# Kernel optimization log

Measured on AMD Instinct MI355X. Metric: run time of the kernel, lower is better.

Reference implementation:

```python
import jax, jax.numpy as jnp
import numpy as np

T, N, L, H, COND, VOCAB = 64, 1024, 16, 256, 64, 100
HC = H + 1  # task_encoder hidden = hidden_size + 1
STATE = 1 + 1 + H + L + L  # a, v, h, a_probs, p


def gru_step(x, h, w_ih, w_hh, b_ih, b_hh):
    # PyTorch GRU/GRUCell gate math
    gi = x @ w_ih.T + b_ih
    gh = h @ w_hh.T + b_hh
    ir, iz, ig = jnp.split(gi, 3, axis=-1)
    hr, hz, hg = jnp.split(gh, 3, axis=-1)
    r = jax.nn.sigmoid(ir + hr)
    z = jax.nn.sigmoid(iz + hz)
    n = jnp.tanh(ig + r * hg)
    return (1.0 - z) * n + z * h


def setup_inputs():
    ks = jax.random.split(jax.random.key(0), 20)
    g = lambda i, sh: jax.random.normal(ks[i], sh, jnp.float32) * 0.05
    return {
        "condition": jax.random.normal(ks[0], (T, N, COND), jnp.float32),
        "lines": jax.random.randint(ks[1], (N, L), 0, VOCAB),
        "actions": jax.random.randint(ks[2], (T, N), 0, L),
        "rnn_hxs": jnp.zeros((N, STATE), jnp.float32),
        "emb": g(3, (VOCAB, H)),
        "w_ih_enc": g(4, (3 * HC, H)), "w_hh_enc": g(5, (3 * HC, HC)),
        "b_ih_enc": g(6, (3 * HC,)), "b_hh_enc": g(7, (3 * HC,)),
        "W1": g(8, (H, COND + H)), "b1": g(9, (H,)),
        "W2": g(10, (H, H)), "b2": g(11, (H,)),
        "w_ih_cell": g(12, (3 * H, H)), "w_hh_cell": g(13, (3 * H, H)),
        "b_ih_cell": g(14, (3 * H,)), "b_hh_cell": g(15, (3 * H,)),
        "Wa": g(16, (H, H)), "ba": g(17, (H,)),
        "Wc": g(18, (1, H)), "bc": g(19, (1,)),
    }


def _forward(condition, rnn_hxs, emb, w_ih_enc, w_hh_enc, b_ih_enc, b_hh_enc,
             W1, b1, W2, b2, w_ih_cell, w_hh_cell, b_ih_cell, b_hh_cell,
             Wa, ba, Wc, bc, lines, actions):
    n, l = lines.shape
    M = emb[lines]                     # [N, L, H]
    seq = jnp.transpose(M, (1, 0, 2))  # [L, N, H]
    idx = jnp.arange(l)

    # backward encoder: single scan over reversed sequence (outputs are causal,
    # so they equal torch's task_encoder(backward_input[:i]) for every i)
    def bstep(h, x):
        h2 = gru_step(x, h, w_ih_enc, w_hh_enc, b_ih_enc, b_hh_enc)
        return h2, h2
    _, B = jax.lax.scan(bstep, jnp.zeros((n, HC), M.dtype), seq[::-1])  # [L, N, HC]

    # forward encoder from every start i, batched over i with a start mask
    def fstep(carry, xj):
        x, j = xj
        h2 = gru_step(x, carry, w_ih_enc, w_hh_enc, b_ih_enc, b_hh_enc)  # [L(i), N, HC]
        h2 = jnp.where((j >= idx)[:, None, None], h2, carry)
        return h2, h2
    _, Fo = jax.lax.scan(fstep, jnp.zeros((l, n, HC), M.dtype), (seq, idx))  # [j, i, N, HC]
    Fo = jnp.transpose(Fo, (1, 0, 2, 3))                                     # [i, j, N, HC]

    # keys[i] = cat(flip(B[:i]), F_i)  ->  entry j<i is B[i-1-j], else forward enc
    bidx = jnp.clip(idx[:, None] - 1 - idx[None, :], 0, l - 1)  # [i, j]
    Kfull = jnp.where((idx[None, :] < idx[:, None])[:, :, None, None], B[bidx], Fo)
    Kfull = jnp.transpose(Kfull, (2, 0, 1, 3))  # [N, i, j, HC]
    K = Kfull[..., :H].sum(axis=1)              # [N, L, H]
    C = Kfull[..., H]                           # [N, i, j]

    _a, _v, h, _ap, p = jnp.split(rnn_hxs, [1, 2, 2 + H, 2 + H + l], axis=-1)
    new_ep = jnp.all(rnn_hxs == 0.0, axis=-1)
    p = p.at[:, 0].set(jnp.where(new_ep, 1.0, p[:, 0]))

    def step(carry, xs):
        h, p = carry
        cond_t, a_t = xs
        r = jnp.einsum('nl,nlh->nh', p, M)
        x = jnp.concatenate([cond_t, r], axis=-1)
        x = jax.nn.relu(x @ W1.T + b1)
        x = jax.nn.relu(x @ W2.T + b2)
        h = gru_step(x, h, w_ih_cell, w_hh_cell, b_ih_cell, b_hh_cell)
        k = h @ Wa.T + ba
        c = jnp.einsum('ni,nij->nj', p, C)
        w = jnp.einsum('nlh,nh->nl', K, k)
        probs = jax.nn.softmax(w * c, axis=-1)
        p_new = jax.nn.one_hot(a_t, l, dtype=h.dtype)  # actions >= 0 -> no resampling
        v = h @ Wc.T + bc
        out = jnp.concatenate([a_t[:, None].astype(h.dtype), v, h, probs, p_new], axis=-1)
        return (h, p_new), out

    _, hx = jax.lax.scan(step, (h, p), (condition, actions))  # [T, N, STATE]
    return hx


def reference(condition, lines, actions, rnn_hxs, emb, w_ih_enc, w_hh_enc, b_ih_enc, b_hh_enc, W1, b1, W2, b2, w_ih_cell, w_hh_cell, b_ih_cell, b_hh_cell, Wa, ba, Wc, bc):
    hx = _forward(condition, rnn_hxs, emb, w_ih_enc, w_hh_enc, b_ih_enc, b_hh_enc,
                  W1, b1, W2, b2, w_ih_cell, w_hh_cell, b_ih_cell, b_hh_cell,
                  Wa, ba, Wc, bc, lines, actions)
    return hx, hx[-1:]
```

## Files before the change

kernel.cpp:

```cpp
#include <hip/hip_runtime.h>
#include <hip/hip_bf16.h>
#include <cstddef>

#define T_ 64
#define N_ 1024
#define L_ 16
#define H_ 256
#define STATE_ 290
#define EKSTR 296

typedef short s16x8 __attribute__((ext_vector_type(8)));
typedef float f32x4 __attribute__((ext_vector_type(4)));
typedef ushort us4 __attribute__((ext_vector_type(4)));
typedef ushort us8 __attribute__((ext_vector_type(8)));
#define MFMA16 __builtin_amdgcn_mfma_f32_16x16x32_bf16

#define BAR() asm volatile("s_waitcnt lgkmcnt(0)\n\ts_barrier" ::: "memory")

__device__ __forceinline__ float b2f(ushort u){ return __uint_as_float(((unsigned)u) << 16); }
__device__ __forceinline__ ushort f2b(float f){
  unsigned x = __float_as_uint(f);
  return (ushort)((x + 0x7FFFu + ((x >> 16) & 1u)) >> 16);
}
__device__ __forceinline__ float gruh(float gir,float giz,float gig,
                                      float ghr,float ghz,float ghg,float hp){
  float r = 1.f/(1.f + __expf(-(gir + ghr)));
  float z = 1.f/(1.f + __expf(-(giz + ghz)));
  float ex = __expf(2.f*(gig + r*ghg));
  float g = 1.f - 2.f/(ex + 1.f);
  return (1.f - z)*g + z*hp;
}

__global__ void prep_all(
    const float* __restrict__ wih_e, const float* __restrict__ whh_e,
    ushort* __restrict__ wihe_p, ushort* __restrict__ whhe_p,
    const float* __restrict__ wih_c, const float* __restrict__ whh_c,
    ushort* __restrict__ wihc_p, ushort* __restrict__ whhc_p,
    const float* __restrict__ bih_c, const float* __restrict__ bhh_c, float* __restrict__ cb,
    const float* __restrict__ W1, ushort* __restrict__ W1b,
    const float* __restrict__ W2, ushort* __restrict__ W2b,
    const float* __restrict__ Wa, ushort* __restrict__ WaTb){
  int b = blockIdx.x, t = threadIdx.x;
  if (b < 832) {
    int idx = b*256 + t;
    int d = idx >> 8, c = idx & 255;
    int tile = d >> 4, uu = d & 15;
    int k = tile/3, p = tile - 3*k;
    int hc = k*16 + uu;
    bool ok = (tile < 51) && (hc < 257);
    wihe_p[idx] = ok ? f2b(wih_e[(size_t)(p*257 + hc)*256 + c]) : (ushort)0;
  } else if (b < 1768) {
    int idx = (b-832)*256 + t;
    int d = idx / 288, c = idx - d*288;
    int tile = d >> 4, uu = d & 15;
    int k = tile/3, p = tile - 3*k;
    int hc = k*16 + uu;
    bool ok = (tile < 51) && (hc < 257) && (c < 257);
    whhe_p[idx] = ok ? f2b(whh_e[(size_t)(p*257 + hc)*257 + c]) : (ushort)0;
  } else if (b < 2536) {
    int idx = (b-1768)*256 + t;
    int d = idx >> 8, c = idx & 255;
    int tile = d >> 4, uu = d & 15;
    int k = tile/3, p = tile - 3*k;
    wihc_p[idx] = f2b(wih_c[(size_t)(p*256 + k*16 + uu)*256 + c]);
  } else if (b < 3304) {
    int idx = (b-2536)*256 + t;
    int d = idx >> 8, c = idx & 255;
    int tile = d >> 4, uu = d & 15;
    int k = tile/3, p = tile - 3*k;
    whhc_p[idx] = f2b(whh_c[(size_t)(p*256 + k*16 + uu)*256 + c]);
  } else if (b < 3307) {
    int d = (b-3304)*256 + t;
    if (d < 768) {
      int tile = d >> 4, uu = d & 15;
      int k = tile/3, p = tile - 3*k;
      int src = p*256 + k*16 + uu;
      cb[d] = bih_c[src] + (p < 2 ? bhh_c[src] : 0.f);
    }
  } else if (b < 3627) {
    int idx = (b-3307)*256 + t;
    W1b[idx] = f2b(W1[idx]);
  } else if (b < 3883) {
    int idx = (b-3627)*256 + t;
    W2b[idx] = f2b(W2[idx]);
  } else {
    int m = b - 3883;
    WaTb[(size_t)t*256 + m] = f2b(Wa[(size_t)m*256 + t]);
  }
}

__global__ void emb_init_r0(
    const int* __restrict__ lines, const float* __restrict__ emb, const float* __restrict__ hxs,
    ushort* __restrict__ Mbf, float* __restrict__ hbuf, float* __restrict__ p0,
    float* __restrict__ r0v){
  __shared__ ushort Ms[16][256];
  __shared__ float p0s[16];
  __shared__ int ls[16];
  __shared__ int nz;
  int n = blockIdx.x, t = threadIdx.x;
  if (t == 0) nz = 0;
  if (t < 16) ls[t] = lines[n*16 + t];
  __syncthreads();
  #pragma unroll
  for (int l = 0; l < 16; ++l) {
    ushort v = f2b(emb[(size_t)ls[l]*256 + t]);
    Ms[l][t] = v;
    Mbf[((size_t)n*16 + l)*256 + t] = v;
  }
  for (int c = t; c < STATE_; c += 256)
    if (hxs[(size_t)n*STATE_ + c] != 0.f) atomicOr(&nz, 1);
  __syncthreads();
  bool new_ep = (nz == 0);
  hbuf[(size_t)n*256 + t] = hxs[(size_t)n*STATE_ + 2 + t];
  if (t < 16) {
    float pv = hxs[(size_t)n*STATE_ + 2 + 256 + 16 + t];
    if (t == 0 && new_ep) pv = 1.f;
    p0[n*16 + t] = pv;
    p0s[t] = pv;
  }
  __syncthreads();
  float s = 0.f;
  #pragma unroll
  for (int l = 0; l < 16; ++l) s += p0s[l]*b2f(Ms[l][t]);
  r0v[(size_t)n*256 + t] = s;
}

__global__ void build_xcat8(const float* __restrict__ cond, const int* __restrict__ act,
                            const float* __restrict__ r0v, const ushort* __restrict__ Mbf,
                            ushort* __restrict__ xcat){
  int idx = blockIdx.x*256 + threadIdx.x;
  if (idx >= T_*N_*40) return;
  int kc = idx % 40;
  int row = idx / 40;
  int n = row & 1023, t = row >> 10;
  us8 v;
  if (kc < 8) {
    const float* cp = cond + (size_t)row*64 + kc*8;
    #pragma unroll
    for (int i = 0; i < 8; ++i) v[i] = f2b(cp[i]);
  } else if (t == 0) {
    const float* rp = r0v + (size_t)n*256 + (kc-8)*8;
    #pragma unroll
    for (int i = 0; i < 8; ++i) v[i] = f2b(rp[i]);
  } else {
    int a = act[(size_t)(t-1)*1024 + n];
    v = *(const us8*)(Mbf + ((size_t)n*16 + a)*256 + (kc-8)*8);
  }
  *(us8*)(xcat + (size_t)idx*8) = v;
}

template<int RELU>
__global__ __launch_bounds__(256) void gemm_mfma(
    const ushort* __restrict__ A, const ushort* __restrict__ W,
    const float* __restrict__ bias, ushort* __restrict__ out,
    int Kd, int ldo){
  __shared__ __align__(16) ushort Ws[64*328];
  int lane = threadIdx.x & 63, wv = threadIdx.x >> 6;
  int u = lane & 15, g4 = lane >> 4;
  int br = blockIdx.x*64 + wv*16;
  int bm = blockIdx.y*64;
  int ldw = Kd + 8;
  for (int i = threadIdx.x; i < 8*Kd; i += 256) {
    int e = i*8;
    int row = e / Kd, col = e - row*Kd;
    *(us8*)&Ws[row*ldw + col] = *(const us8*)(W + (size_t)(bm + row)*Kd + col);
  }
  __syncthreads();
  const ushort* Arow = A + (size_t)(br + u)*Kd + g4*8;
  f32x4 acc0 = {0,0,0,0}, acc1 = {0,0,0,0}, acc2 = {0,0,0,0}, acc3 = {0,0,0,0};
  for (int k0 = 0; k0 < Kd; k0 += 32) {
    s16x8 av = *(const s16x8*)(Arow + k0);
    s16x8 b0 = *(const s16x8*)&Ws[( 0 + u)*ldw + k0 + g4*8];
    s16x8 b1 = *(const s16x8*)&Ws[(16 + u)*ldw + k0 + g4*8];
    s16x8 b2 = *(const s16x8*)&Ws[(32 + u)*ldw + k0 + g4*8];
    s16x8 b3 = *(const s16x8*)&Ws[(48 + u)*ldw + k0 + g4*8];
    acc0 = MFMA16(av, b0, acc0, 0,0,0);
    acc1 = MFMA16(av, b1, acc1, 0,0,0);
    acc2 = MFMA16(av, b2, acc2, 0,0,0);
    acc3 = MFMA16(av, b3, acc3, 0,0,0);
  }
  f32x4 ac[4] = {acc0, acc1, acc2, acc3};
  #pragma unroll
  for (int mt = 0; mt < 4; ++mt) {
    int col = bm + mt*16 + u;
    float b = bias ? bias[col] : 0.f;
    #pragma unroll
    for (int r = 0; r < 4; ++r) {
      float v = ac[mt][r] + b;
      if (RELU) v = fmaxf(v, 0.f);
      out[(size_t)(br + g4*4 + r)*ldo + col] = f2b(v);
    }
  }
}

__global__ __launch_bounds__(512) __attribute__((amdgpu_waves_per_eu(2, 2))) void enc_all(
    const ushort* __restrict__ GiAll, const ushort* __restrict__ Wh,
    const float* __restrict__ bih, const float* __restrict__ bhh,
    float* __restrict__ Km, float* __restrict__ Cm, ushort* __restrict__ Bbf){
  __shared__ __align__(16) ushort hbf[2][80][EKSTR];
  __shared__ __align__(16) ushort gis[2][2][4][832];
  int tid = threadIdx.x, lane = tid & 63, wv = tid >> 6;
  int u = lane & 15, g4 = lane >> 4;
  int nb = blockIdx.x * 4;
  for (int i = tid; i < 2*80*EKSTR; i += 512) ((ushort*)hbf)[i] = 0;
  #pragma unroll
  for (int i0 = 0; i0 < 4; ++i0) {
    int i = tid + i0*512;
    if (i < 1664) {
      int flat = i*4;
      int fb = flat / 3328, rem = flat - fb*3328;
      int nl = rem / 832, k = rem - nl*832;
      int row = (nb+nl)*16 + (fb ? 15 : 0);
      *(us4*)&gis[0][fb][nl][k] = *(const us4*)(GiAll + (size_t)row*832 + k);
    }
  }
  BAR();
  int cur = 0;
  for (int j = 0; j < 16; ++j) {
    if (j < 15) {
      #pragma unroll
      for (int i0 = 0; i0 < 4; ++i0) {
        int i = tid + i0*512;
        if (i < 1664) {
          int flat = i*4;
          int fb = flat / 3328, rem = flat - fb*3328;
          int nl = rem / 832, k = rem - nl*832;
          int row = (nb+nl)*16 + (fb ? (14-j) : (j+1));
          *(us4*)&gis[cur^1][fb][nl][k] = *(const us4*)(GiAll + (size_t)row*832 + k);
        }
      }
    }
    #pragma unroll 1
    for (int tt = 0; tt < 2; ++tt) {
      int kt = 2*wv + tt;
      f32x4 acc[5][3];
      #pragma unroll
      for (int rt = 0; rt < 5; ++rt) {
        acc[rt][0] = (f32x4){0,0,0,0};
        acc[rt][1] = (f32x4){0,0,0,0};
        acc[rt][2] = (f32x4){0,0,0,0};
      }
      #pragma unroll
      for (int q = 0; q < 9; ++q) {
        int off = q*32 + g4*8;
        s16x8 w0 = *(const s16x8*)(Wh + (size_t)((3*kt+0)*16 + u)*288 + off);
        s16x8 w1 = *(const s16x8*)(Wh + (size_t)((3*kt+1)*16 + u)*288 + off);
        s16x8 w2 = *(const s16x8*)(Wh + (size_t)((3*kt+2)*16 + u)*288 + off);
        #pragma unroll
        for (int rt = 0; rt < 5; ++rt) {
          if (rt < 4 && rt*4 > j) continue;
          s16x8 av = *(const s16x8*)&hbf[cur][rt*16 + u][off];
          acc[rt][0] = MFMA16(av, w0, acc[rt][0], 0,0,0);
          acc[rt][1] = MFMA16(av, w1, acc[rt][1], 0,0,0);
          acc[rt][2] = MFMA16(av, w2, acc[rt][2], 0,0,0);
        }
      }
      int c = kt*16 + u;
      float bi0 = bih[c], bi1 = bih[257+c], bi2 = bih[514+c];
      float bh0 = bhh[c], bh1 = bhh[257+c], bh2 = bhh[514+c];
      float kmP[4] = {0.f, 0.f, 0.f, 0.f};
      #pragma unroll
      for (int rt = 0; rt < 4; ++rt) {
        int ii = rt*4 + g4;
        if (rt*4 <= j && ii <= j) {
          #pragma unroll
          for (int r = 0; r < 4; ++r) {
            int rowl = rt*16 + g4*4 + r;
            const ushort* gp = &gis[cur][0][r][3*kt*16];
            float hp = b2f(hbf[cur][rowl][c]);
            float h2 = gruh(b2f(gp[u]) + bi0, b2f(gp[16+u]) + bi1, b2f(gp[32+u]) + bi2,
                            acc[rt][0][r] + bh0, acc[rt][1][r] + bh1,
                            acc[rt][2][r] + bh2, hp);
            hbf[cur^1][rowl][c] = f2b(h2);
            kmP[r] += h2;
          }
        }
      }
      #pragma unroll
      for (int r = 0; r < 4; ++r) {
        float s = kmP[r];
        s += __shfl_xor(s, 16, 64);
        s += __shfl_xor(s, 32, 64);
        if (g4 == 0) Km[((size_t)(nb+r)*16 + j)*256 + c] = s;
      }
      if (g4 == 0) {
        #pragma unroll
        for (int r = 0; r < 4; ++r) {
          const ushort* gp = &gis[cur][1][r][3*kt*16];
          float hp = b2f(hbf[cur][64 + r][c]);
          float h2 = gruh(b2f(gp[u]) + bi0, b2f(gp[16+u]) + bi1, b2f(gp[32+u]) + bi2,
                          acc[4][0][r] + bh0, acc[4][1][r] + bh1,
                          acc[4][2][r] + bh2, hp);
          hbf[cur^1][64 + r][c] = f2b(h2);
          Bbf[((size_t)j*1024 + nb + r)*288 + c] = f2b(h2);
        }
      }
    }
    if (wv < 5) {
      int rt = wv;
      bool go = (rt == 4) || (rt*4 <= j);
      if (go) {
        f32x4 a0 = {0,0,0,0}, a1 = {0,0,0,0}, a2 = {0,0,0,0};
        #pragma unroll
        for (int q = 0; q < 9; ++q) {
          int off = q*32 + g4*8;
          s16x8 w0 = *(const s16x8*)(Wh + (size_t)(48*16 + u)*288 + off);
          s16x8 w1 = *(const s16x8*)(Wh + (size_t)(49*16 + u)*288 + off);
          s16x8 w2 = *(const s16x8*)(Wh + (size_t)(50*16 + u)*288 + off);
          s16x8 av = *(const s16x8*)&hbf[cur][rt*16 + u][off];
          a0 = MFMA16(av, w0, a0, 0,0,0);
          a1 = MFMA16(av, w1, a1, 0,0,0);
          a2 = MFMA16(av, w2, a2, 0,0,0);
        }
        if (u == 0) {
          float bi0 = bih[256], bi1 = bih[513], bi2 = bih[770];
          float bh0 = bhh[256], bh1 = bhh[513], bh2 = bhh[770];
          if (rt < 4) {
            int ii = rt*4 + g4;
            if (ii <= j) {
              #pragma unroll
              for (int r = 0; r < 4; ++r) {
                int rowl = rt*16 + g4*4 + r;
                const ushort* gp = &gis[cur][0][r][768];
                float hp = b2f(hbf[cur][rowl][256]);
                float h2 = gruh(b2f(gp[0]) + bi0, b2f(gp[16]) + bi1, b2f(gp[32]) + bi2,
                                a0[r] + bh0, a1[r] + bh1, a2[r] + bh2, hp);
                hbf[cur^1][rowl][256] = f2b(h2);
                Cm[(size_t)(nb+r)*256 + ii*16 + j] = h2;
              }
            }
          } else if (g4 == 0) {
            #pragma unroll
            for (int r = 0; r < 4; ++r) {
              const ushort* gp = &gis[cur][1][r][768];
              float hp = b2f(hbf[cur][64 + r][256]);
              float h2 = gruh(b2f(gp[0]) + bi0, b2f(gp[16]) + bi1, b2f(gp[32]) + bi2,
                              a0[r] + bh0, a1[r] + bh1, a2[r] + bh2, hp);
              hbf[cur^1][64 + r][256] = f2b(h2);
              Bbf[((size_t)j*1024 + nb + r)*288 + 256] = f2b(h2);
            }
          }
        }
      }
    }
    BAR();
    cur ^= 1;
  }
}

__global__ void accum_wb(const ushort* __restrict__ Bbf, const float* __restrict__ Km,
                         ushort* __restrict__ Kmbf, float* __restrict__ Cm,
                         const float* __restrict__ ba, float* __restrict__ wbv){
  __shared__ float kms[16][257];
  int n = blockIdx.x, c = threadIdx.x;
  float s = 0.f;
  for (int jj = 15; jj >= 0; --jj) {
    if (jj < 15) s += b2f(Bbf[((size_t)(14-jj)*1024 + n)*288 + c]);
    size_t o = ((size_t)n*16 + jj)*256 + c;
    float v = Km[o] + s;
    Kmbf[o] = f2b(v);
    kms[jj][c] = v;
  }
  int i = c >> 4, j = c & 15;
  if (i > j) Cm[(size_t)n*256 + i*16 + j] = b2f(Bbf[((size_t)(i-1-j)*1024 + n)*288 + 256]);
  __syncthreads();
  int l = c >> 4, lane16 = c & 15;
  float t = 0.f;
  for (int m = lane16; m < 256; m += 16) t += kms[l][m]*ba[m];
  t += __shfl_down(t, 8, 16); t += __shfl_down(t, 4, 16);
  t += __shfl_down(t, 2, 16); t += __shfl_down(t, 1, 16);
  if (lane16 == 0) wbv[n*16 + l] = t;
}

__global__ __launch_bounds__(512) __attribute__((amdgpu_waves_per_eu(2, 2))) void cell_chunk(
    const ushort* __restrict__ Gi, const ushort* __restrict__ Wh,
    const float* __restrict__ bhh, const float* __restrict__ hbuf,
    int t0, ushort* __restrict__ hcT, float* __restrict__ out){
  __shared__ __align__(16) ushort hbf[2][16][266];
  __shared__ __align__(16) ushort gis[2][16][768];
  int tid = threadIdx.x, lane = tid & 63, wv = tid >> 6;
  int u = lane & 15, g4 = lane >> 4;
  int n0 = blockIdx.x * 16;
  int ktA = wv, ktB = wv + 8;
  int cA = ktA*16 + u, cB = ktB*16 + u;
  s16x8 WA0[8], WA1[8], WA2[8], WB0[8], WB1[8], WB2[8];
  #pragma unroll
  for (int q = 0; q < 8; ++q) {
    int off = q*32 + g4*8;
    WA0[q] = *(const s16x8*)(Wh + (size_t)((3*ktA+0)*16 + u)*256 + off);
    WA1[q] = *(const s16x8*)(Wh + (size_t)((3*ktA+1)*16 + u)*256 + off);
    WA2[q] = *(const s16x8*)(Wh + (size_t)((3*ktA+2)*16 + u)*256 + off);
    WB0[q] = *(const s16x8*)(Wh + (size_t)((3*ktB+0)*16 + u)*256 + off);
    WB1[q] = *(const s16x8*)(Wh + (size_t)((3*ktB+1)*16 + u)*256 + off);
    WB2[q] = *(const s16x8*)(Wh + (size_t)((3*ktB+2)*16 + u)*256 + off);
  }
  float bhgA = bhh[512 + cA], bhgB = bhh[512 + cB];
  if (t0 == 0) {
    for (int i = tid; i < 16*256; i += 512) {
      int rr = i >> 8, cc = i & 255;
      hbf[0][rr][cc] = f2b(hbuf[(size_t)(n0 + rr)*256 + cc]);
    }
  } else {
    for (int i = tid; i < 16*256; i += 512) {
      int rr = i >> 8, cc = i & 255;
      hbf[0][rr][cc] = hcT[((size_t)(t0-1)*1024 + n0 + rr)*256 + cc];
    }
  }
  for (int i = tid; i < 1536; i += 512)
    *(us8*)&((ushort*)gis[0])[i*8] = *(const us8*)(Gi + (size_t)n0*768 + i*8);
  BAR();
  int cur = 0;
  for (int s = 0; s < 16; ++s) {
    int t = t0 + s;
    if (s < 15) {
      const ushort* src = Gi + (size_t)(s+1)*1024*768 + (size_t)n0*768;
      for (int i = tid; i < 1536; i += 512)
        *(us8*)&((ushort*)gis[cur^1])[i*8] = *(const us8*)(src + i*8);
    }
    f32x4 a0={0,0,0,0},a1={0,0,0,0},a2={0,0,0,0};
    f32x4 b0={0,0,0,0},b1={0,0,0,0},b2={0,0,0,0};
    #pragma unroll
    for (int q = 0; q < 8; ++q) {
      s16x8 ah = *(const s16x8*)&hbf[cur][u][q*32 + g4*8];
      a0 = MFMA16(ah, WA0[q], a0, 0,0,0);
      a1 = MFMA16(ah, WA1[q], a1, 0,0,0);
      a2 = MFMA16(ah, WA2[q], a2, 0,0,0);
      b0 = MFMA16(ah, WB0[q], b0, 0,0,0);
      b1 = MFMA16(ah, WB1[q], b1, 0,0,0);
      b2 = MFMA16(ah, WB2[q], b2, 0,0,0);
    }
    #pragma unroll
    for (int r = 0; r < 4; ++r) {
      int row = g4*4 + r;
      const ushort* gr = &gis[cur][row][0];
      {
        float gir = b2f(gr[3*ktA*16 + u]);
        float giz = b2f(gr[3*ktA*16 + 16 + u]);
        float gig = b2f(gr[3*ktA*16 + 32 + u]);
        float hp  = b2f(hbf[cur][row][cA]);
        float rr2 = 1.f/(1.f + __expf(-(gir + a0[r])));
        float zz  = 1.f/(1.f + __expf(-(giz + a1[r])));
        float ex  = __expf(2.f*(gig + rr2*(a2[r] + bhgA)));
        float gg  = 1.f - 2.f/(ex + 1.f);
        float h2  = (1.f - zz)*gg + zz*hp;
        ushort hb = f2b(h2);
        hbf[cur^1][row][cA] = hb;
        hcT[((size_t)t*1024 + n0 + row)*256 + cA] = hb;
        out[((size_t)t*1024 + n0 + row)*STATE_ + 2 + cA] = h2;
        if (t == 63) out[((size_t)64*1024 + n0 + row)*STATE_ + 2 + cA] = h2;
      }
      {
        float gir = b2f(gr[3*ktB*16 + u]);
        float giz = b2f(gr[3*ktB*16 + 16 + u]);
        float gig = b2f(gr[3*ktB*16 + 32 + u]);
        float hp  = b2f(hbf[cur][row][cB]);
        float rr2 = 1.f/(1.f + __expf(-(gir + b0[r])));
        float zz  = 1.f/(1.f + __expf(-(giz + b1[r])));
        float ex  = __expf(2.f*(gig + rr2*(b2[r] + bhgB)));
        float gg  = 1.f - 2.f/(ex + 1.f);
        float h2  = (1.f - zz)*gg + zz*hp;
        ushort hb = f2b(h2);
        hbf[cur^1][row][cB] = hb;
        hcT[((size_t)t*1024 + n0 + row)*256 + cB] = hb;
        out[((size_t)t*1024 + n0 + row)*STATE_ + 2 + cB] = h2;
        if (t == 63) out[((size_t)64*1024 + n0 + row)*STATE_ + 2 + cB] = h2;
      }
    }
    BAR();
    cur ^= 1;
  }
}

__global__ __launch_bounds__(256) void attn_v(
    const ushort* __restrict__ Ktl, const ushort* __restrict__ hcT,
    const float* __restrict__ wbv, const float* __restrict__ Cm,
    const float* __restrict__ p0, const int* __restrict__ act,
    const float* __restrict__ Wc, const float* __restrict__ bc,
    float* __restrict__ out){
  __shared__ float WcS[256];
  int n = blockIdx.x;
  int tid = threadIdx.x;
  WcS[tid] = Wc[tid];
  __syncthreads();
  int lane = tid & 63, wv = tid >> 6;
  int u = lane & 15, g4 = lane >> 4;
  int t0 = wv*16;
  const ushort* Ka = Ktl + ((size_t)n*16 + u)*256 + g4*8;
  const ushort* Hb = hcT + ((size_t)(t0 + u)*1024 + n)*256 + g4*8;
  f32x4 acc = {0,0,0,0};
  float vp = 0.f;
  #pragma unroll
  for (int q = 0; q < 8; ++q) {
    s16x8 av = *(const s16x8*)(Ka + q*32);
    s16x8 bv = *(const s16x8*)(Hb + q*32);
    acc = MFMA16(av, bv, acc, 0,0,0);
    #pragma unroll
    for (int j = 0; j < 8; ++j) vp += b2f((ushort)bv[j]) * WcS[q*32 + g4*8 + j];
  }
  vp += __shfl_xor(vp, 16, 64);
  vp += __shfl_xor(vp, 32, 64);
  float vfin = vp + bc[0];
  int t = t0 + u;
  float ps[4];
  if (t == 0) {
    #pragma unroll
    for (int r = 0; r < 4; ++r) {
      float catt = 0.f;
      for (int i = 0; i < 16; ++i) catt += p0[n*16 + i]*Cm[(size_t)n*256 + i*16 + g4*4 + r];
      ps[r] = (acc[r] + wbv[n*16 + g4*4 + r]) * catt;
    }
  } else {
    int ap = act[(size_t)(t-1)*1024 + n];
    #pragma unroll
    for (int r = 0; r < 4; ++r)
      ps[r] = (acc[r] + wbv[n*16 + g4*4 + r]) * Cm[(size_t)n*256 + ap*16 + g4*4 + r];
  }
  float mx = fmaxf(fmaxf(ps[0], ps[1]), fmaxf(ps[2], ps[3]));
  mx = fmaxf(mx, __shfl_xor(mx, 16, 64));
  mx = fmaxf(mx, __shfl_xor(mx, 32, 64));
  float e[4], se = 0.f;
  #pragma unroll
  for (int r = 0; r < 4; ++r) { e[r] = __expf(ps[r] - mx); se += e[r]; }
  se += __shfl_xor(se, 16, 64);
  se += __shfl_xor(se, 32, 64);
  float inv = 1.f/se;
  int a = act[(size_t)t*1024 + n];
  size_t ro = ((size_t)t*1024 + n)*STATE_;
  if (g4 == 0) { out[ro] = (float)a; out[ro + 1] = vfin; }
  #pragma unroll
  for (int r = 0; r < 4; ++r) {
    out[ro + 258 + g4*4 + r] = e[r]*inv;
    out[ro + 274 + g4*4 + r] = (g4*4 + r == a) ? 1.f : 0.f;
  }
  if (t == 63) {
    size_t r2 = ((size_t)64*1024 + n)*STATE_;
    if (g4 == 0) { out[r2] = (float)a; out[r2 + 1] = vfin; }
    #pragma unroll
    for (int r = 0; r < 4; ++r) {
      out[r2 + 258 + g4*4 + r] = e[r]*inv;
      out[r2 + 274 + g4*4 + r] = (g4*4 + r == a) ? 1.f : 0.f;
    }
  }
}

extern "C" void kernel_launch(void* const* d_in, const int* in_sizes, int n_in,
                              void* d_out, int out_size, void* d_ws, size_t ws_size,
                              hipStream_t stream){
  (void)in_sizes; (void)n_in; (void)out_size; (void)ws_size;
  const float* cond  = (const float*)d_in[0];
  const int*   lines = (const int*)  d_in[1];
  const int*   act   = (const int*)  d_in[2];
  const float* hxs   = (const float*)d_in[3];
  const float* emb   = (const float*)d_in[4];
  const float* wih_e = (const float*)d_in[5];
  const float* whh_e = (const float*)d_in[6];
  const float* bih_e = (const float*)d_in[7];
  const float* bhh_e = (const float*)d_in[8];
  const float* W1    = (const float*)d_in[9];
  const float* b1    = (const float*)d_in[10];
  const float* W2    = (const float*)d_in[11];
  const float* b2    = (const float*)d_in[12];
  const float* wih_c = (const float*)d_in[13];
  const float* whh_c = (const float*)d_in[14];
  const float* bih_c = (const float*)d_in[15];
  const float* bhh_c = (const float*)d_in[16];
  const float* Wa    = (const float*)d_in[17];
  const float* ba    = (const float*)d_in[18];
  const float* Wc    = (const float*)d_in[19];
  const float* bc    = (const float*)d_in[20];
  float* out = (float*)d_out;

  char* base = (char*)d_ws;
  ushort* Mbf    = (ushort*)(base + 0);
  ushort* Bbf    = (ushort*)(base + 8388608);
  float*  Km     = (float*) (base + 17825792);
  ushort* Kmbf   = (ushort*)(base + 34603008);
  ushort* xcat   = (ushort*)(base + 8388608);
  ushort* x2     = (ushort*)(base + 8388608);
  ushort* hcT    = (ushort*)(base + 8388608);
  ushort* GiAll  = (ushort*)(base + 50331648);
  ushort* x1     = (ushort*)(base + 50331648);
  ushort* GiC0   = (ushort*)(base + 50331648);
  ushort* GiC1   = (ushort*)(base + 75497472);
  ushort* Ktl    = (ushort*)(base + 100663296);
  float*  Cm     = (float*) (base + 109051904);
  float*  hbuf   = (float*) (base + 110100480);
  float*  p0     = (float*) (base + 111149056);
  float*  r0v    = (float*) (base + 111214592);
  float*  wbv    = (float*) (base + 112263168);
  ushort* wihe_p = (ushort*)(base + 112328704);
  ushort* whhe_p = (ushort*)(base + 112754688);
  ushort* wihc_p = (ushort*)(base + 113233920);
  ushort* whhc_p = (ushort*)(base + 113627136);
  ushort* W1b    = (ushort*)(base + 114020352);
  ushort* W2b    = (ushort*)(base + 114184192);
  ushort* WaTb   = (ushort*)(base + 114315264);
  float*  cbias  = (float*) (base + 114446336);

  prep_all<<<4139, 256, 0, stream>>>(wih_e, whh_e, wihe_p, whhe_p,
                                     wih_c, whh_c, wihc_p, whhc_p,
                                     bih_c, bhh_c, cbias, W1, W1b, W2, W2b, Wa, WaTb);
  emb_init_r0<<<1024, 256, 0, stream>>>(lines, emb, hxs, Mbf, hbuf, p0, r0v);

  gemm_mfma<0><<<dim3(256, 13), 256, 0, stream>>>(Mbf, wihe_p, nullptr, GiAll, 256, 832);
  enc_all<<<256, 512, 0, stream>>>(GiAll, whhe_p, bih_e, bhh_e, Km, Cm, Bbf);
  accum_wb<<<1024, 256, 0, stream>>>(Bbf, Km, Kmbf, Cm, ba, wbv);
  gemm_mfma<0><<<dim3(256, 4), 256, 0, stream>>>(Kmbf, WaTb, nullptr, Ktl, 256, 256);

  build_xcat8<<<10240, 256, 0, stream>>>(cond, act, r0v, Mbf, xcat);
  gemm_mfma<1><<<dim3(1024, 4), 256, 0, stream>>>(xcat, W1b, b1, x1, 320, 256);
  gemm_mfma<1><<<dim3(1024, 4), 256, 0, stream>>>(x1, W2b, b2, x2, 256, 256);

  ushort* gic[2] = {GiC0, GiC1};
  gemm_mfma<0><<<dim3(256, 12), 256, 0, stream>>>(x2 + (size_t)0*16384*256, wihc_p, cbias, gic[0], 256, 768);
  gemm_mfma<0><<<dim3(256, 12), 256, 0, stream>>>(x2 + (size_t)1*16384*256, wihc_p, cbias, gic[1], 256, 768);
  cell_chunk<<<64, 512, 0, stream>>>(gic[0], whhc_p, bhh_c, hbuf,  0, hcT, out);
  gemm_mfma<0><<<dim3(256, 12), 256, 0, stream>>>(x2 + (size_t)2*16384*256, wihc_p, cbias, gic[0], 256, 768);
  cell_chunk<<<64, 512, 0, stream>>>(gic[1], whhc_p, bhh_c, hbuf, 16, hcT, out);
  gemm_mfma<0><<<dim3(256, 12), 256, 0, stream>>>(x2 + (size_t)3*16384*256, wihc_p, cbias, gic[1], 256, 768);
  cell_chunk<<<64, 512, 0, stream>>>(gic[0], whhc_p, bhh_c, hbuf, 32, hcT, out);
  cell_chunk<<<64, 512, 0, stream>>>(gic[1], whhc_p, bhh_c, hbuf, 48, hcT, out);

  attn_v<<<1024, 256, 0, stream>>>(Ktl, hcT, wbv, Cm, p0, act, Wc, bc, out);
}
```

Before: 886.2 us.

## Halve sequences per encoder block and double grid for higher occupancy

The forward/backward encoder kernel now processes 2 sequences per block instead of 4, launching 512 blocks instead of 256. Shared-memory buffers and accumulator tiles shrink, and the rows are remapped so two sequences interleave inside each 16-row MFMA tile. Waves-per-EU is raised from 2 to 4 so more blocks can be resident, improving latency hiding and CU coverage on the serial 16-step recurrence. The cost is that each recurrent weight load is amortised over fewer rows, which increases total weight traffic.

```diff
diff --git a/kernel.cpp b/kernel.cpp
--- a/kernel.cpp
+++ b/kernel.cpp
@@ -193,22 +193,22 @@
   }
 }
 
-__global__ __launch_bounds__(512) __attribute__((amdgpu_waves_per_eu(2, 2))) void enc_all(
+__global__ __launch_bounds__(512) __attribute__((amdgpu_waves_per_eu(4, 4))) void enc_all(
     const ushort* __restrict__ GiAll, const ushort* __restrict__ Wh,
     const float* __restrict__ bih, const float* __restrict__ bhh,
     float* __restrict__ Km, float* __restrict__ Cm, ushort* __restrict__ Bbf){
-  __shared__ __align__(16) ushort hbf[2][80][EKSTR];
-  __shared__ __align__(16) ushort gis[2][2][4][832];
+  __shared__ __align__(16) ushort hbf[2][48][EKSTR];
+  __shared__ __align__(16) ushort gis[2][2][2][832];
   int tid = threadIdx.x, lane = tid & 63, wv = tid >> 6;
   int u = lane & 15, g4 = lane >> 4;
-  int nb = blockIdx.x * 4;
-  for (int i = tid; i < 2*80*EKSTR; i += 512) ((ushort*)hbf)[i] = 0;
-  #pragma unroll
-  for (int i0 = 0; i0 < 4; ++i0) {
-    int i = tid + i0*512;
-    if (i < 1664) {
-      int flat = i*4;
-      int fb = flat / 3328, rem = flat - fb*3328;
+  int nb = blockIdx.x * 2;
+  for (int i = tid; i < 2*48*EKSTR; i += 512) ((ushort*)hbf)[i] = 0;
+  #pragma unroll
+  for (int s2 = 0; s2 < 2; ++s2) {
+    int ch = tid + s2*512;
+    if (ch < 832) {
+      int e = ch*4;
+      int fb = e / 1664, rem = e - fb*1664;
       int nl = rem / 832, k = rem - nl*832;
       int row = (nb+nl)*16 + (fb ? 15 : 0);
       *(us4*)&gis[0][fb][nl][k] = *(const us4*)(GiAll + (size_t)row*832 + k);
@@ -219,11 +219,11 @@
   for (int j = 0; j < 16; ++j) {
     if (j < 15) {
       #pragma unroll
-      for (int i0 = 0; i0 < 4; ++i0) {
-        int i = tid + i0*512;
-        if (i < 1664) {
-          int flat = i*4;
-          int fb = flat / 3328, rem = flat - fb*3328;
+      for (int s2 = 0; s2 < 2; ++s2) {
+        int ch = tid + s2*512;
+        if (ch < 832) {
+          int e = ch*4;
+          int fb = e / 1664, rem = e - fb*1664;
           int nl = rem / 832, k = rem - nl*832;
           int row = (nb+nl)*16 + (fb ? (14-j) : (j+1));
           *(us4*)&gis[cur^1][fb][nl][k] = *(const us4*)(GiAll + (size_t)row*832 + k);
@@ -233,9 +233,9 @@
     #pragma unroll 1
     for (int tt = 0; tt < 2; ++tt) {
       int kt = 2*wv + tt;
-      f32x4 acc[5][3];
+      f32x4 acc[3][3];
       #pragma unroll
-      for (int rt = 0; rt < 5; ++rt) {
+      for (int rt = 0; rt < 3; ++rt) {
         acc[rt][0] = (f32x4){0,0,0,0};
         acc[rt][1] = (f32x4){0,0,0,0};
         acc[rt][2] = (f32x4){0,0,0,0};
@@ -247,8 +247,8 @@
         s16x8 w1 = *(const s16x8*)(Wh + (size_t)((3*kt+1)*16 + u)*288 + off);
         s16x8 w2 = *(const s16x8*)(Wh + (size_t)((3*kt+2)*16 + u)*288 + off);
         #pragma unroll
-        for (int rt = 0; rt < 5; ++rt) {
-          if (rt < 4 && rt*4 > j) continue;
+        for (int rt = 0; rt < 3; ++rt) {
+          if (rt < 2 && rt*8 > j) continue;
           s16x8 av = *(const s16x8*)&hbf[cur][rt*16 + u][off];
           acc[rt][0] = MFMA16(av, w0, acc[rt][0], 0,0,0);
           acc[rt][1] = MFMA16(av, w1, acc[rt][1], 0,0,0);
@@ -258,47 +258,51 @@
       int c = kt*16 + u;
       float bi0 = bih[c], bi1 = bih[257+c], bi2 = bih[514+c];
       float bh0 = bhh[c], bh1 = bhh[257+c], bh2 = bhh[514+c];
-      float kmP[4] = {0.f, 0.f, 0.f, 0.f};
+      float kmP[2] = {0.f, 0.f};
       #pragma unroll
-      for (int rt = 0; rt < 4; ++rt) {
-        int ii = rt*4 + g4;
-        if (rt*4 <= j && ii <= j) {
+      for (int rt = 0; rt < 2; ++rt) {
+        if (rt*8 <= j) {
           #pragma unroll
           for (int r = 0; r < 4; ++r) {
-            int rowl = rt*16 + g4*4 + r;
-            const ushort* gp = &gis[cur][0][r][3*kt*16];
-            float hp = b2f(hbf[cur][rowl][c]);
-            float h2 = gruh(b2f(gp[u]) + bi0, b2f(gp[16+u]) + bi1, b2f(gp[32+u]) + bi2,
-                            acc[rt][0][r] + bh0, acc[rt][1][r] + bh1,
-                            acc[rt][2][r] + bh2, hp);
-            hbf[cur^1][rowl][c] = f2b(h2);
-            kmP[r] += h2;
+            int i = rt*8 + g4*2 + (r >> 1);
+            int nl = r & 1;
+            if (i <= j) {
+              int rowl = rt*16 + g4*4 + r;
+              const ushort* gp = &gis[cur][0][nl][3*kt*16];
+              float hp = b2f(hbf[cur][rowl][c]);
+              float h2 = gruh(b2f(gp[u]) + bi0, b2f(gp[16+u]) + bi1, b2f(gp[32+u]) + bi2,
+                              acc[rt][0][r] + bh0, acc[rt][1][r] + bh1,
+                              acc[rt][2][r] + bh2, hp);
+              hbf[cur^1][rowl][c] = f2b(h2);
+              kmP[nl] += h2;
+            }
           }
         }
       }
-      #pragma unroll
-      for (int r = 0; r < 4; ++r) {
-        float s = kmP[r];
-        s += __shfl_xor(s, 16, 64);
-        s += __shfl_xor(s, 32, 64);
-        if (g4 == 0) Km[((size_t)(nb+r)*16 + j)*256 + c] = s;
+      kmP[0] += __shfl_xor(kmP[0], 16, 64);
+      kmP[0] += __shfl_xor(kmP[0], 32, 64);
+      kmP[1] += __shfl_xor(kmP[1], 16, 64);
+      kmP[1] += __shfl_xor(kmP[1], 32, 64);
+      if (g4 == 0) {
+        Km[((size_t)(nb+0)*16 + j)*256 + c] = kmP[0];
+        Km[((size_t)(nb+1)*16 + j)*256 + c] = kmP[1];
       }
       if (g4 == 0) {
         #pragma unroll
-        for (int r = 0; r < 4; ++r) {
-          const ushort* gp = &gis[cur][1][r][3*kt*16];
-          float hp = b2f(hbf[cur][64 + r][c]);
+        for (int nl = 0; nl < 2; ++nl) {
+          const ushort* gp = &gis[cur][1][nl][3*kt*16];
+          float hp = b2f(hbf[cur][32 + nl][c]);
           float h2 = gruh(b2f(gp[u]) + bi0, b2f(gp[16+u]) + bi1, b2f(gp[32+u]) + bi2,
-                          acc[4][0][r] + bh0, acc[4][1][r] + bh1,
-                          acc[4][2][r] + bh2, hp);
-          hbf[cur^1][64 + r][c] = f2b(h2);
-          Bbf[((size_t)j*1024 + nb + r)*288 + c] = f2b(h2);
+                          acc[2][0][nl] + bh0, acc[2][1][nl] + bh1,
+                          acc[2][2][nl] + bh2, hp);
+          hbf[cur^1][32 + nl][c] = f2b(h2);
+          Bbf[((size_t)j*1024 + nb + nl)*288 + c] = f2b(h2);
         }
       }
     }
-    if (wv < 5) {
+    if (wv < 3) {
       int rt = wv;
-      bool go = (rt == 4) || (rt*4 <= j);
+      bool go = (rt == 2) || (rt*8 <= j);
       if (go) {
         f32x4 a0 = {0,0,0,0}, a1 = {0,0,0,0}, a2 = {0,0,0,0};
         #pragma unroll
@@ -315,29 +319,30 @@
         if (u == 0) {
           float bi0 = bih[256], bi1 = bih[513], bi2 = bih[770];
           float bh0 = bhh[256], bh1 = bhh[513], bh2 = bhh[770];
-          if (rt < 4) {
-            int ii = rt*4 + g4;
-            if (ii <= j) {
-              #pragma unroll
-              for (int r = 0; r < 4; ++r) {
+          if (rt < 2) {
+            #pragma unroll
+            for (int r = 0; r < 4; ++r) {
+              int i = rt*8 + g4*2 + (r >> 1);
+              int nl = r & 1;
+              if (i <= j) {
                 int rowl = rt*16 + g4*4 + r;
-                const ushort* gp = &gis[cur][0][r][768];
+                const ushort* gp = &gis[cur][0][nl][768];
                 float hp = b2f(hbf[cur][rowl][256]);
                 float h2 = gruh(b2f(gp[0]) + bi0, b2f(gp[16]) + bi1, b2f(gp[32]) + bi2,
                                 a0[r] + bh0, a1[r] + bh1, a2[r] + bh2, hp);
                 hbf[cur^1][rowl][256] = f2b(h2);
-                Cm[(size_t)(nb+r)*256 + ii*16 + j] = h2;
+                Cm[(size_t)(nb+nl)*256 + i*16 + j] = h2;
               }
             }
           } else if (g4 == 0) {
             #pragma unroll
-            for (int r = 0; r < 4; ++r) {
-              const ushort* gp = &gis[cur][1][r][768];
-              float hp = b2f(hbf[cur][64 + r][256]);
+            for (int nl = 0; nl < 2; ++nl) {
+              const ushort* gp = &gis[cur][1][nl][768];
+              float hp = b2f(hbf[cur][32 + nl][256]);
               float h2 = gruh(b2f(gp[0]) + bi0, b2f(gp[16]) + bi1, b2f(gp[32]) + bi2,
-                              a0[r] + bh0, a1[r] + bh1, a2[r] + bh2, hp);
-              hbf[cur^1][64 + r][256] = f2b(h2);
-              Bbf[((size_t)j*1024 + nb + r)*288 + 256] = f2b(h2);
+                              a0[nl] + bh0, a1[nl] + bh1, a2[nl] + bh2, hp);
+              hbf[cur^1][32 + nl][256] = f2b(h2);
+              Bbf[((size_t)j*1024 + nb + nl)*288 + 256] = f2b(h2);
             }
           }
         }
@@ -603,7 +608,7 @@
   emb_init_r0<<<1024, 256, 0, stream>>>(lines, emb, hxs, Mbf, hbuf, p0, r0v);
 
   gemm_mfma<0><<<dim3(256, 13), 256, 0, stream>>>(Mbf, wihe_p, nullptr, GiAll, 256, 832);
-  enc_all<<<256, 512, 0, stream>>>(GiAll, whhe_p, bih_e, bhh_e, Km, Cm, Bbf);
+  enc_all<<<512, 512, 0, stream>>>(GiAll, whhe_p, bih_e, bhh_e, Km, Cm, Bbf);
   accum_wb<<<1024, 256, 0, stream>>>(Bbf, Km, Kmbf, Cm, ba, wbv);
   gemm_mfma<0><<<dim3(256, 4), 256, 0, stream>>>(Kmbf, WaTb, nullptr, Ktl, 256, 256);
 
```

Measured after the change: 941.4 us. 1.06x slower.
